# Kernel tuning notes

Measured on AMD Instinct MI355X. Metric: run time of the kernel, lower is better.

## Reference

```python
import jax, jax.numpy as jnp
import numpy as np
import math

EPS = 1e-7
N, M, K, D_IN, D_OUT = 8192, 32, 8, 64, 64
KP_EXTENT = 0.66

# ---- Lorentz manifold (curvature k = 1) helpers ----

def l_inner(x, y):
    # Lorentzian inner product, keepdim on last axis
    return -x[..., :1] * y[..., :1] + jnp.sum(x[..., 1:] * y[..., 1:], axis=-1, keepdims=True)

def l_dist(x, y):
    alpha = jnp.clip(-l_inner(x, y), 1.0 + EPS, None)
    return jnp.arccosh(alpha)[..., 0]

def expmap0(u):
    # u: tangent at origin, time component ignored-by-construction (zero)
    sp = u[..., 1:]
    un = jnp.sqrt(jnp.clip(jnp.sum(sp * sp, axis=-1, keepdims=True), 1e-14, None))
    return jnp.concatenate([jnp.cosh(un), jnp.sinh(un) * sp / un], axis=-1)

def expmap(x, u):
    un = jnp.sqrt(jnp.clip(l_inner(u, u), 1e-14, None))
    return jnp.cosh(un) * x + jnp.sinh(un) * u / un

def logmap(x, y):
    alpha = jnp.clip(-l_inner(x, y), 1.0 + EPS, None)
    d = jnp.arccosh(alpha)
    nom = y - alpha * x
    den = jnp.sqrt(jnp.clip(alpha * alpha - 1.0, 1e-14, None))
    return d * nom / den

def ptransp(x, y, v):
    # parallel transport of v from x to y
    return v + l_inner(y, v) / (1.0 - l_inner(x, y)) * (x + y)

def norm_midpoint(ave):
    den = jnp.sqrt(jnp.clip(jnp.abs(l_inner(ave, ave)), 1e-8, None))
    return ave / den


def setup_inputs() -> dict:
    key = jax.random.key(0)
    k1, k2, k3, k4, k5, k6 = jax.random.split(key, 6)
    # points on the hyperboloid: time = sqrt(1 + ||space||^2)
    sp = jax.random.normal(k1, (N, D_IN - 1), dtype=jnp.float32) * 0.5
    t = jnp.sqrt(1.0 + jnp.sum(sp * sp, axis=-1, keepdims=True))
    x = jnp.concatenate([t, sp], axis=-1)
    nei = jax.random.randint(k2, (N, M), 0, N, dtype=jnp.int32)
    nei_mask = jax.random.randint(k3, (N, M), 0, 2, dtype=jnp.int32)
    # kernel points: tangent vectors at origin (time comp 0), first point = center
    kp_sp = jax.random.normal(k4, (K, D_IN - 1), dtype=jnp.float32)
    kp_sp = kp_sp / jnp.linalg.norm(kp_sp, axis=-1, keepdims=True)
    radii = jax.random.uniform(k5, (K, 1), dtype=jnp.float32) * KP_EXTENT
    kp_sp = kp_sp * radii
    kp_sp = kp_sp.at[0].set(0.0)
    kernel_points = jnp.concatenate([jnp.zeros((K, 1), jnp.float32), kp_sp], axis=-1)
    # K LorentzLinear params
    stdv = 1.0 / math.sqrt(D_OUT)
    W = jax.random.uniform(k6, (K, D_OUT, D_IN), dtype=jnp.float32, minval=-stdv, maxval=stdv)
    W = W.at[:, :, 0].set(0.0)  # reset_parameters zeros first input column
    b = jnp.zeros((K, D_OUT), dtype=jnp.float32)
    scale = jnp.full((K,), math.log(10.0), dtype=jnp.float32)
    return {"x": x, "nei": nei, "nei_mask": nei_mask, "W": W, "b": b,
            "scale": scale, "kernel_points": kernel_points}


def reference(x, nei, nei_mask, W, b, scale, kernel_points):
    n, d = x.shape
    x_nei = x[nei]                      # [n, m, d] gather
    xr = x[:, None, :]                  # [n, 1, d]
    og_row = jnp.zeros((d,), x.dtype).at[0].set(1.0)
    # transport_x: map each neighborhood to the origin's tangent frame
    v = logmap(xr, x_nei)
    x0_nei = expmap0(ptransp(xr, og_row[None, None, :], v))   # [n, m, d]
    # kernel positions at the origin (transp=True => base point is origin)
    tmp = expmap(og_row[None, :], ptransp(og_row[None, :], og_row[None, :], kernel_points[1:]))
    x_kernel = jnp.concatenate([tmp, og_row[None, :]], axis=0)  # [K, d]
    # geodesic distances neighbor <-> kernel point: [n, K, m]
    dis = l_dist(x0_nei[:, None, :, :], x_kernel[None, :, None, :])
    dis = dis * nei_mask[:, None, :].astype(x.dtype)
    # K LorentzLinear transforms (vectorized over K): [n, K, m, d_out]
    h = jnp.einsum('nmd,kod->nkmo', x0_nei, W) + b[None, :, None, :]
    time = jax.nn.sigmoid(h[..., :1]) * jnp.exp(scale)[None, :, None, None] + 1.0001
    nar = h[..., 1:]
    s = (time * time - 1.0) / jnp.clip(jnp.sum(nar * nar, axis=-1, keepdims=True), 1e-8, None)
    xt = jnp.concatenate([time, nar * jnp.sqrt(s)], axis=-1)
    # weighted Lorentz midpoint over kernel points, per neighbor: [n, m, d_out]
    per_nei = norm_midpoint(jnp.einsum('nkm,nkmo->nmo', dis, xt))
    # unweighted Lorentz midpoint over neighbors: [n, d_out]
    return norm_midpoint(per_nei.mean(axis=1))
```

## Files before the change

### kernel.cpp

```cpp
#include <hip/hip_runtime.h>
#include <hip/hip_bf16.h>

#define N_NODES 8192
#define M_NEI   32
#define K_PTS   8
#define D       64
#define EPS_    1e-7f

typedef float f4v __attribute__((ext_vector_type(4)));
typedef short s8v __attribute__((ext_vector_type(8)));

__device__ __forceinline__ ushort f2bf(float f) {
  __hip_bfloat16 h = __float2bfloat16(f);
  return *reinterpret_cast<ushort*>(&h);
}
__device__ __forceinline__ float bf2f(ushort u) {
  __hip_bfloat16 h;
  *reinterpret_cast<ushort*>(&h) = u;
  return __bfloat162float(h);
}
__device__ __forceinline__ float frcp(float x)  { return __builtin_amdgcn_rcpf(x); }
__device__ __forceinline__ float frsq(float x)  { return __builtin_amdgcn_rsqf(x); }
__device__ __forceinline__ float fsqrt(float x) { return __builtin_amdgcn_sqrtf(x); }
__device__ __forceinline__ float facosh(float a) {
  float den = fsqrt(fmaxf(a * a - 1.f, 1e-14f));
  return __logf(a + den);
}

template<int CTRL>
__device__ __forceinline__ float dppadd(float v) {
  int t = __builtin_amdgcn_update_dpp(0, __float_as_int(v), CTRL, 0xf, 0xf, true);
  return v + __int_as_float(t);
}
template<int CTRL>
__device__ __forceinline__ float dppmov(float v) {
  return __int_as_float(__builtin_amdgcn_update_dpp(0, __float_as_int(v), CTRL, 0xf, 0xf, true));
}
__device__ __forceinline__ float swz_xor4(float v) {
  return __int_as_float(__builtin_amdgcn_ds_swizzle(__float_as_int(v), 0x101F));
}
__device__ __forceinline__ float sum8(float v) {
  v = dppadd<0xB1>(v);
  v = dppadd<0x4E>(v);
  v = dppadd<0x141>(v);
  return v;
}
__device__ __forceinline__ float sum16(float v) {
  v = dppadd<0x121>(v);
  v = dppadd<0x122>(v);
  v = dppadd<0x124>(v);
  v = dppadd<0x128>(v);
  return v;
}

__global__ void prep_xk(const float* __restrict__ kp, const float* __restrict__ scale,
                        float* __restrict__ xk) {
  int d = threadIdx.x;
  for (int kk = 0; kk < K_PTS - 1; ++kk) {
    float v = kp[(kk + 1) * D + d];
    float p = (d == 0) ? 0.f : v * v;
    #pragma unroll
    for (int s = 1; s < 64; s <<= 1) p += __shfl_xor(p, s);
    float un = sqrtf(fmaxf(p, 1e-14f));
    float sh = sinhf(un) / un;
    xk[kk * D + d] = (d == 0) ? coshf(un) : sh * v;
  }
  xk[(K_PTS - 1) * D + d] = (d == 0) ? 1.f : 0.f;
  if (d < K_PTS) xk[K_PTS * D + d] = expf(scale[d]);
}

__global__ void prep_wb(const float* __restrict__ W, ushort* __restrict__ WF) {
  int idx = blockIdx.x * 256 + threadIdx.x;
  int k    = idx >> 9;
  int ct   = (idx >> 7) & 3;
  int ks   = (idx >> 6) & 1;
  int lane = idx & 63;
  int o  = ct * 16 + (lane & 15);
  int db = (lane >> 4) * 8 + ks * 32;
  const float* wrow = W + (k * 64 + o) * 64 + db;
  s8v hi, lo;
  #pragma unroll
  for (int j = 0; j < 8; ++j) {
    float w = wrow[j];
    ushort h = f2bf(w);
    hi[j] = (short)h;
    lo[j] = (short)f2bf(w - bf2f(h));
  }
  int f = (k * 4 + ct) * 2 + ks;
  *(s8v*)(WF + (size_t)(f * 2 + 0) * 512 + lane * 8) = hi;
  *(s8v*)(WF + (size_t)(f * 2 + 1) * 512 + lane * 8) = lo;
}

__launch_bounds__(256, 4)
__global__ void kpa_main(const float* __restrict__ x, const int* __restrict__ nei,
                         const int* __restrict__ mask, const ushort* __restrict__ WF,
                         const float* __restrict__ b, const float* __restrict__ scale,
                         const float* __restrict__ xk, float* __restrict__ out) {
  __shared__ __align__(16) float  xr_s[D];
  __shared__ __align__(16) float  xk_s[K_PTS * D];
  __shared__ __align__(16) ushort Ah_lds[M_NEI * D];
  __shared__ __align__(16) ushort Al_lds[M_NEI * D];
  __shared__ float dis_s[K_PTS * 33];
  __shared__ __align__(8)  float  hss[K_PTS * M_NEI * 2];
  __shared__ __align__(16) float  red_h[2][16 * 68];
  __shared__ __align__(16) float  redp2[2][64];

  const int n  = blockIdx.x;
  const int t  = threadIdx.x;
  const int w4 = t >> 6;
  const int l  = t & 63;
  const int cl = l & 15;
  const int gr = l >> 4;
  const int wm = w4 & 1;
  const int wk = w4 >> 1;

  if (t < D) xr_s[t] = x[n * D + t];
  xk_s[t] = xk[t]; xk_s[t + 256] = xk[t + 256];
  __syncthreads();

  {
    const int m  = t >> 3;
    const int l8 = t & 7;
    const int d0 = l8 * 8;
    const int ni = nei[n * M_NEI + m];
    float y[8], xr[8];
    float y0 = x[ni * D];
    {
      float4 ya = *(const float4*)(x + ni * D + d0);
      float4 yb = *(const float4*)(x + ni * D + d0 + 4);
      y[0]=ya.x; y[1]=ya.y; y[2]=ya.z; y[3]=ya.w;
      y[4]=yb.x; y[5]=yb.y; y[6]=yb.z; y[7]=yb.w;
      float4 ra = *(const float4*)(xr_s + d0);
      float4 rb = *(const float4*)(xr_s + d0 + 4);
      xr[0]=ra.x; xr[1]=ra.y; xr[2]=ra.z; xr[3]=ra.w;
      xr[4]=rb.x; xr[5]=rb.y; xr[6]=rb.z; xr[7]=rb.w;
    }
    const float xr0 = xr_s[0];
    float p = 0.f;
    #pragma unroll
    for (int j = 0; j < 8; ++j) p += xr[j] * y[j];
    if (l8 == 0) p -= 2.f * xr[0] * y[0];
    p = sum8(p);
    float alpha = fmaxf(-p, 1.f + EPS_);
    float den = fsqrt(fmaxf(alpha * alpha - 1.f, 1e-14f));
    float dd  = __logf(alpha + den);
    float f   = dd * frcp(den);
    float v[8];
    #pragma unroll
    for (int j = 0; j < 8; ++j) v[j] = f * (y[j] - alpha * xr[j]);
    float v0 = f * (y0 - alpha * xr0);
    float c  = -v0 * frcp(1.f + xr0);
    float wv[8];
    float q = 0.f;
    #pragma unroll
    for (int j = 0; j < 8; ++j) { wv[j] = v[j] + c * xr[j]; q += wv[j] * wv[j]; }
    if (l8 == 0) q -= wv[0] * wv[0];
    q = sum8(q);
    float un = fsqrt(fmaxf(q, 1e-14f));
    float e  = __expf(un);
    float ei = frcp(e);
    float sh = (0.5f * (e - ei)) * frcp(un);
    float x0v[8];
    #pragma unroll
    for (int j = 0; j < 8; ++j) x0v[j] = sh * wv[j];
    if (l8 == 0) x0v[0] = 0.5f * (e + ei);
    {
      s8v hi, lo;
      #pragma unroll
      for (int j = 0; j < 8; ++j) {
        uint u = __float_as_uint(x0v[j]);
        hi[j] = (short)(ushort)(u >> 16);
        float lof = x0v[j] - __uint_as_float(u & 0xffff0000u);
        uint ul = __float_as_uint(lof);
        lo[j] = (short)(ushort)((ul + 0x7fffu + ((ul >> 16) & 1u)) >> 16);
      }
      int byte = m * 128 + d0 * 2;
      int swz  = byte ^ ((m & 7) << 4);
      *(s8v*)((char*)Ah_lds + swz) = hi;
      *(s8v*)((char*)Al_lds + swz) = lo;
    }
    float msk = (float)mask[n * M_NEI + m];
    if (l8 == 0) x0v[0] = -x0v[0];
    float pk[8];
    #pragma unroll
    for (int kk = 0; kk < K_PTS; ++kk) {
      const float* xkp = xk_s + kk * D + d0;
      float pp = 0.f;
      #pragma unroll
      for (int j = 0; j < 8; ++j) pp += x0v[j] * xkp[j];
      pk[kk] = pp;
    }
    const bool hi4 = (l8 & 4);
    float s1[4];
    #pragma unroll
    for (int j = 0; j < 4; ++j) {
      float give = hi4 ? pk[j] : pk[j + 4];
      float keep = hi4 ? pk[j + 4] : pk[j];
      s1[j] = keep + swz_xor4(give);
    }
    const bool hi2 = (l8 & 2);
    float s2[2];
    #pragma unroll
    for (int j = 0; j < 2; ++j) {
      float give = hi2 ? s1[j] : s1[j + 2];
      float keep = hi2 ? s1[j + 2] : s1[j];
      s2[j] = keep + dppmov<0x4E>(give);
    }
    const bool hi1 = (l8 & 1);
    float give = hi1 ? s2[0] : s2[1];
    float keep = hi1 ? s2[1] : s2[0];
    float mypp = keep + dppmov<0xB1>(give);
    float al_ = fmaxf(-mypp, 1.f + EPS_);
    dis_s[l8 * 33 + m] = facosh(al_) * msk;
  }
  __syncthreads();

  const int row = wm * 16 + cl;
  s8v ah[2], alo[2];
  #pragma unroll
  for (int ks = 0; ks < 2; ++ks) {
    int byte = row * 128 + (gr * 8 + ks * 32) * 2;
    int swz  = byte ^ ((row & 7) << 4);
    ah[ks]  = *(const s8v*)((const char*)Ah_lds + swz);
    alo[ks] = *(const s8v*)((const char*)Al_lds + swz);
  }

  f4v acc[4][4];
  #pragma unroll
  for (int kq = 0; kq < 4; ++kq) {
    const int k = wk * 4 + kq;
    #pragma unroll
    for (int ct = 0; ct < 4; ++ct) {
      float bv = b[k * 64 + ct * 16 + cl];
      f4v a = (f4v){bv, bv, bv, bv};
      #pragma unroll
      for (int ks = 0; ks < 2; ++ks) {
        int fi = (k * 4 + ct) * 2 + ks;
        s8v bh = *(const s8v*)(WF + (size_t)(fi * 2 + 0) * 512 + l * 8);
        s8v bl = *(const s8v*)(WF + (size_t)(fi * 2 + 1) * 512 + l * 8);
        a = __builtin_amdgcn_mfma_f32_16x16x32_bf16(ah[ks],  bh, a, 0, 0, 0);
        a = __builtin_amdgcn_mfma_f32_16x16x32_bf16(ah[ks],  bl, a, 0, 0, 0);
        a = __builtin_amdgcn_mfma_f32_16x16x32_bf16(alo[ks], bh, a, 0, 0, 0);
      }
      acc[kq][ct] = a;
    }
    #pragma unroll
    for (int r = 0; r < 4; ++r) {
      float ss = acc[kq][0][r]*acc[kq][0][r] + acc[kq][1][r]*acc[kq][1][r]
               + acc[kq][2][r]*acc[kq][2][r] + acc[kq][3][r]*acc[kq][3][r];
      ss = sum16(ss);
      if (cl == 0) {
        const int m = wm * 16 + gr * 4 + r;
        *(float2*)&hss[(k * M_NEI + m) * 2] = make_float2(acc[kq][0][r], ss);
      }
    }
  }
  __syncthreads();

  {
    const int k = t >> 5;
    const int m = t & 31;
    float2 hp = *(const float2*)&hss[(k * M_NEI + m) * 2];
    float h0 = hp.x, ss = hp.y;
    float nar2 = fmaxf(ss - h0 * h0, 1e-8f);
    float es   = xk[K_PTS * D + k];
    float time = es * frcp(1.f + __expf(-h0)) + 1.0001f;
    float sq   = fsqrt(time * time - 1.f) * frsq(nar2);
    float dm   = dis_s[k * 33 + m];
    *(float2*)&hss[(k * M_NEI + m) * 2] = make_float2(dm * sq, dm * time);
  }
  __syncthreads();

  float yacc[4][4];
  #pragma unroll
  for (int r = 0; r < 4; ++r)
    #pragma unroll
    for (int ct = 0; ct < 4; ++ct) yacc[r][ct] = 0.f;

  #pragma unroll
  for (int kq = 0; kq < 4; ++kq) {
    const int k = wk * 4 + kq;
    #pragma unroll
    for (int r = 0; r < 4; ++r) {
      const int m = wm * 16 + gr * 4 + r;
      float2 dd = *(const float2*)&hss[(k * M_NEI + m) * 2];
      yacc[r][0] += (cl == 0) ? dd.y : dd.x * acc[kq][0][r];
      yacc[r][1] += dd.x * acc[kq][1][r];
      yacc[r][2] += dd.x * acc[kq][2][r];
      yacc[r][3] += dd.x * acc[kq][3][r];
    }
  }

  if (wk == 1) {
    #pragma unroll
    for (int r = 0; r < 4; ++r) {
      const int ml = gr * 4 + r;
      float* rw = &red_h[wm][ml * 68];
      rw[cl]      = yacc[r][0];
      rw[16 + cl] = yacc[r][1];
      rw[32 + cl] = yacc[r][2];
      rw[48 + cl] = yacc[r][3];
    }
  }
  __syncthreads();

  if (wk == 0) {
    float s[4] = {0.f, 0.f, 0.f, 0.f};
    #pragma unroll
    for (int r = 0; r < 4; ++r) {
      const int ml = gr * 4 + r;
      const float* rw = &red_h[wm][ml * 68];
      float v0_ = yacc[r][0] + rw[cl];
      float v1_ = yacc[r][1] + rw[16 + cl];
      float v2_ = yacc[r][2] + rw[32 + cl];
      float v3_ = yacc[r][3] + rw[48 + cl];
      float ip = v0_*v0_ + v1_*v1_ + v2_*v2_ + v3_*v3_;
      if (cl == 0) ip -= 2.f * v0_ * v0_;
      ip = sum16(ip);
      float rin = frsq(fmaxf(fabsf(ip), 1e-8f));
      s[0] += v0_ * rin; s[1] += v1_ * rin;
      s[2] += v2_ * rin; s[3] += v3_ * rin;
    }
    #pragma unroll
    for (int j = 0; j < 4; ++j) {
      float z = s[j];
      z += __shfl_xor(z, 16); z += __shfl_xor(z, 32);
      s[j] = z;
    }
    if (gr == 0) {
      #pragma unroll
      for (int j = 0; j < 4; ++j) redp2[wm][j * 16 + cl] = s[j];
    }
  }
  __syncthreads();

  if (t < 16) {
    float mv[4]; float ip = 0.f;
    #pragma unroll
    for (int j = 0; j < 4; ++j) {
      mv[j] = (redp2[0][j * 16 + t] + redp2[1][j * 16 + t]) * (1.f / 32.f);
      ip += mv[j] * mv[j];
    }
    if (t == 0) ip -= 2.f * mv[0] * mv[0];
    ip = sum16(ip);
    float rin = frsq(fmaxf(fabsf(ip), 1e-8f));
    #pragma unroll
    for (int j = 0; j < 4; ++j) out[n * D + j * 16 + t] = mv[j] * rin;
  }
}

extern "C" void kernel_launch(void* const* d_in, const int* in_sizes, int n_in,
                              void* d_out, int out_size, void* d_ws, size_t ws_size,
                              hipStream_t stream) {
  const float* x     = (const float*)d_in[0];
  const int*   nei   = (const int*)d_in[1];
  const int*   mask  = (const int*)d_in[2];
  const float* W     = (const float*)d_in[3];
  const float* b     = (const float*)d_in[4];
  const float* scale = (const float*)d_in[5];
  const float* kp    = (const float*)d_in[6];
  float* out = (float*)d_out;

  ushort* WF = (ushort*)d_ws;
  float*  xk = (float*)(WF + 65536);

  prep_wb<<<16, 256, 0, stream>>>(W, WF);
  prep_xk<<<1, 64, 0, stream>>>(kp, scale, xk);
  kpa_main<<<N_NODES, 256, 0, stream>>>(x, nei, mask, WF, b, scale, xk, out);
}
```

Baseline: 103.0 us.

## Add per-kernel-point streamed variant with higher occupancy bound and runtime selection

Adds a second main kernel that processes the four kernel points per wave one at a time (non-unrolled loop) instead of holding all sixteen MFMA accumulators live. This lets it use launch bounds of 5 blocks per CU instead of 4. The host checks whether the new kernel compiled without register spills and launches it if so, otherwise falls back to the original. The trade is more occupancy against a serialized per-k loop that has less instruction-level parallelism. Each launch now also makes an extra host-side attribute query.

```diff
diff --git a/kernel.cpp b/kernel.cpp
--- a/kernel.cpp
+++ b/kernel.cpp
@@ -91,11 +91,168 @@
   *(s8v*)(WF + (size_t)(f * 2 + 1) * 512 + lane * 8) = lo;
 }
 
+#define KPA_PROLOGUE_AND_DIS                                                        \
+  if (t < D) xr_s[t] = x[n * D + t];                                                \
+  xk_s[t] = xk[t]; xk_s[t + 256] = xk[t + 256];                                     \
+  __syncthreads();                                                                  \
+  {                                                                                 \
+    const int m  = t >> 3;                                                          \
+    const int l8 = t & 7;                                                           \
+    const int d0 = l8 * 8;                                                          \
+    const int ni = nei[n * M_NEI + m];                                              \
+    float y[8], xr[8];                                                              \
+    float y0 = x[ni * D];                                                           \
+    {                                                                               \
+      float4 ya = *(const float4*)(x + ni * D + d0);                                \
+      float4 yb = *(const float4*)(x + ni * D + d0 + 4);                            \
+      y[0]=ya.x; y[1]=ya.y; y[2]=ya.z; y[3]=ya.w;                                   \
+      y[4]=yb.x; y[5]=yb.y; y[6]=yb.z; y[7]=yb.w;                                   \
+      float4 ra = *(const float4*)(xr_s + d0);                                      \
+      float4 rb = *(const float4*)(xr_s + d0 + 4);                                  \
+      xr[0]=ra.x; xr[1]=ra.y; xr[2]=ra.z; xr[3]=ra.w;                               \
+      xr[4]=rb.x; xr[5]=rb.y; xr[6]=rb.z; xr[7]=rb.w;                               \
+    }                                                                               \
+    const float xr0 = xr_s[0];                                                      \
+    float p = 0.f;                                                                  \
+    _Pragma("unroll")                                                               \
+    for (int j = 0; j < 8; ++j) p += xr[j] * y[j];                                  \
+    if (l8 == 0) p -= 2.f * xr[0] * y[0];                                           \
+    p = sum8(p);                                                                    \
+    float alpha = fmaxf(-p, 1.f + EPS_);                                            \
+    float den = fsqrt(fmaxf(alpha * alpha - 1.f, 1e-14f));                          \
+    float dd  = __logf(alpha + den);                                                \
+    float f   = dd * frcp(den);                                                     \
+    float v[8];                                                                     \
+    _Pragma("unroll")                                                               \
+    for (int j = 0; j < 8; ++j) v[j] = f * (y[j] - alpha * xr[j]);                  \
+    float v0 = f * (y0 - alpha * xr0);                                              \
+    float c  = -v0 * frcp(1.f + xr0);                                               \
+    float wv[8];                                                                    \
+    float q = 0.f;                                                                  \
+    _Pragma("unroll")                                                               \
+    for (int j = 0; j < 8; ++j) { wv[j] = v[j] + c * xr[j]; q += wv[j] * wv[j]; }   \
+    if (l8 == 0) q -= wv[0] * wv[0];                                                \
+    q = sum8(q);                                                                    \
+    float un = fsqrt(fmaxf(q, 1e-14f));                                             \
+    float e  = __expf(un);                                                          \
+    float ei = frcp(e);                                                             \
+    float sh = (0.5f * (e - ei)) * frcp(un);                                        \
+    float x0v[8];                                                                   \
+    _Pragma("unroll")                                                               \
+    for (int j = 0; j < 8; ++j) x0v[j] = sh * wv[j];                                \
+    if (l8 == 0) x0v[0] = 0.5f * (e + ei);                                          \
+    {                                                                               \
+      s8v hi, lo;                                                                   \
+      _Pragma("unroll")                                                             \
+      for (int j = 0; j < 8; ++j) {                                                 \
+        uint u = __float_as_uint(x0v[j]);                                           \
+        hi[j] = (short)(ushort)(u >> 16);                                           \
+        float lof = x0v[j] - __uint_as_float(u & 0xffff0000u);                      \
+        uint ul = __float_as_uint(lof);                                             \
+        lo[j] = (short)(ushort)((ul + 0x7fffu + ((ul >> 16) & 1u)) >> 16);          \
+      }                                                                             \
+      int byte = m * 128 + d0 * 2;                                                  \
+      int swz  = byte ^ ((m & 7) << 4);                                             \
+      *(s8v*)((char*)Ah_lds + swz) = hi;                                            \
+      *(s8v*)((char*)Al_lds + swz) = lo;                                            \
+    }                                                                               \
+    float msk = (float)mask[n * M_NEI + m];                                         \
+    if (l8 == 0) x0v[0] = -x0v[0];                                                  \
+    float pk[8];                                                                    \
+    _Pragma("unroll")                                                               \
+    for (int kk = 0; kk < K_PTS; ++kk) {                                            \
+      const float* xkp = xk_s + kk * D + d0;                                        \
+      float pp = 0.f;                                                               \
+      _Pragma("unroll")                                                             \
+      for (int j = 0; j < 8; ++j) pp += x0v[j] * xkp[j];                            \
+      pk[kk] = pp;                                                                  \
+    }                                                                               \
+    const bool hi4 = (l8 & 4);                                                      \
+    float s1[4];                                                                    \
+    _Pragma("unroll")                                                               \
+    for (int j = 0; j < 4; ++j) {                                                   \
+      float give = hi4 ? pk[j] : pk[j + 4];                                         \
+      float keep = hi4 ? pk[j + 4] : pk[j];                                         \
+      s1[j] = keep + swz_xor4(give);                                                \
+    }                                                                               \
+    const bool hi2 = (l8 & 2);                                                      \
+    float s2[2];                                                                    \
+    _Pragma("unroll")                                                               \
+    for (int j = 0; j < 2; ++j) {                                                   \
+      float give = hi2 ? s1[j] : s1[j + 2];                                         \
+      float keep = hi2 ? s1[j + 2] : s1[j];                                         \
+      s2[j] = keep + dppmov<0x4E>(give);                                            \
+    }                                                                               \
+    const bool hi1 = (l8 & 1);                                                      \
+    float give = hi1 ? s2[0] : s2[1];                                               \
+    float keep = hi1 ? s2[1] : s2[0];                                               \
+    float mypp = keep + dppmov<0xB1>(give);                                         \
+    float al_ = fmaxf(-mypp, 1.f + EPS_);                                           \
+    dis_s[l8 * 33 + m] = facosh(al_) * msk;                                         \
+  }                                                                                 \
+  __syncthreads();
+
+#define KPA_EPILOGUE                                                                \
+  if (wk == 1) {                                                                    \
+    _Pragma("unroll")                                                               \
+    for (int r = 0; r < 4; ++r) {                                                   \
+      const int ml = gr * 4 + r;                                                    \
+      float* rw = &red_h[wm][ml * 68];                                              \
+      rw[cl]      = yacc[r][0];                                                     \
+      rw[16 + cl] = yacc[r][1];                                                     \
+      rw[32 + cl] = yacc[r][2];                                                     \
+      rw[48 + cl] = yacc[r][3];                                                     \
+    }                                                                               \
+  }                                                                                 \
+  __syncthreads();                                                                  \
+  if (wk == 0) {                                                                    \
+    float s[4] = {0.f, 0.f, 0.f, 0.f};                                              \
+    _Pragma("unroll")                                                               \
+    for (int r = 0; r < 4; ++r) {                                                   \
+      const int ml = gr * 4 + r;                                                    \
+      const float* rw = &red_h[wm][ml * 68];                                        \
+      float v0_ = yacc[r][0] + rw[cl];                                              \
+      float v1_ = yacc[r][1] + rw[16 + cl];                                         \
+      float v2_ = yacc[r][2] + rw[32 + cl];                                         \
+      float v3_ = yacc[r][3] + rw[48 + cl];                                         \
+      float ip = v0_*v0_ + v1_*v1_ + v2_*v2_ + v3_*v3_;                             \
+      if (cl == 0) ip -= 2.f * v0_ * v0_;                                           \
+      ip = sum16(ip);                                                               \
+      float rin = frsq(fmaxf(fabsf(ip), 1e-8f));                                    \
+      s[0] += v0_ * rin; s[1] += v1_ * rin;                                         \
+      s[2] += v2_ * rin; s[3] += v3_ * rin;                                         \
+    }                                                                               \
+    _Pragma("unroll")                                                               \
+    for (int j = 0; j < 4; ++j) {                                                   \
+      float z = s[j];                                                               \
+      z += __shfl_xor(z, 16); z += __shfl_xor(z, 32);                               \
+      s[j] = z;                                                                     \
+    }                                                                               \
+    if (gr == 0) {                                                                  \
+      _Pragma("unroll")                                                             \
+      for (int j = 0; j < 4; ++j) redp2[wm][j * 16 + cl] = s[j];                    \
+    }                                                                               \
+  }                                                                                 \
+  __syncthreads();                                                                  \
+  if (t < 16) {                                                                     \
+    float mv[4]; float ip = 0.f;                                                    \
+    _Pragma("unroll")                                                               \
+    for (int j = 0; j < 4; ++j) {                                                   \
+      mv[j] = (redp2[0][j * 16 + t] + redp2[1][j * 16 + t]) * (1.f / 32.f);         \
+      ip += mv[j] * mv[j];                                                          \
+    }                                                                               \
+    if (t == 0) ip -= 2.f * mv[0] * mv[0];                                          \
+    ip = sum16(ip);                                                                 \
+    float rin = frsq(fmaxf(fabsf(ip), 1e-8f));                                      \
+    _Pragma("unroll")                                                               \
+    for (int j = 0; j < 4; ++j) out[n * D + j * 16 + t] = mv[j] * rin;              \
+  }
+
 __launch_bounds__(256, 4)
-__global__ void kpa_main(const float* __restrict__ x, const int* __restrict__ nei,
-                         const int* __restrict__ mask, const ushort* __restrict__ WF,
-                         const float* __restrict__ b, const float* __restrict__ scale,
-                         const float* __restrict__ xk, float* __restrict__ out) {
+__global__ void kpa_main4(const float* __restrict__ x, const int* __restrict__ nei,
+                          const int* __restrict__ mask, const ushort* __restrict__ WF,
+                          const float* __restrict__ b, const float* __restrict__ scale,
+                          const float* __restrict__ xk, float* __restrict__ out) {
   __shared__ __align__(16) float  xr_s[D];
   __shared__ __align__(16) float  xk_s[K_PTS * D];
   __shared__ __align__(16) ushort Ah_lds[M_NEI * D];
@@ -114,106 +271,7 @@
   const int wm = w4 & 1;
   const int wk = w4 >> 1;
 
-  if (t < D) xr_s[t] = x[n * D + t];
-  xk_s[t] = xk[t]; xk_s[t + 256] = xk[t + 256];
-  __syncthreads();
-
-  {
-    const int m  = t >> 3;
-    const int l8 = t & 7;
-    const int d0 = l8 * 8;
-    const int ni = nei[n * M_NEI + m];
-    float y[8], xr[8];
-    float y0 = x[ni * D];
-    {
-      float4 ya = *(const float4*)(x + ni * D + d0);
-      float4 yb = *(const float4*)(x + ni * D + d0 + 4);
-      y[0]=ya.x; y[1]=ya.y; y[2]=ya.z; y[3]=ya.w;
-      y[4]=yb.x; y[5]=yb.y; y[6]=yb.z; y[7]=yb.w;
-      float4 ra = *(const float4*)(xr_s + d0);
-      float4 rb = *(const float4*)(xr_s + d0 + 4);
-      xr[0]=ra.x; xr[1]=ra.y; xr[2]=ra.z; xr[3]=ra.w;
-      xr[4]=rb.x; xr[5]=rb.y; xr[6]=rb.z; xr[7]=rb.w;
-    }
-    const float xr0 = xr_s[0];
-    float p = 0.f;
-    #pragma unroll
-    for (int j = 0; j < 8; ++j) p += xr[j] * y[j];
-    if (l8 == 0) p -= 2.f * xr[0] * y[0];
-    p = sum8(p);
-    float alpha = fmaxf(-p, 1.f + EPS_);
-    float den = fsqrt(fmaxf(alpha * alpha - 1.f, 1e-14f));
-    float dd  = __logf(alpha + den);
-    float f   = dd * frcp(den);
-    float v[8];
-    #pragma unroll
-    for (int j = 0; j < 8; ++j) v[j] = f * (y[j] - alpha * xr[j]);
-    float v0 = f * (y0 - alpha * xr0);
-    float c  = -v0 * frcp(1.f + xr0);
-    float wv[8];
-    float q = 0.f;
-    #pragma unroll
-    for (int j = 0; j < 8; ++j) { wv[j] = v[j] + c * xr[j]; q += wv[j] * wv[j]; }
-    if (l8 == 0) q -= wv[0] * wv[0];
-    q = sum8(q);
-    float un = fsqrt(fmaxf(q, 1e-14f));
-    float e  = __expf(un);
-    float ei = frcp(e);
-    float sh = (0.5f * (e - ei)) * frcp(un);
-    float x0v[8];
-    #pragma unroll
-    for (int j = 0; j < 8; ++j) x0v[j] = sh * wv[j];
-    if (l8 == 0) x0v[0] = 0.5f * (e + ei);
-    {
-      s8v hi, lo;
-      #pragma unroll
-      for (int j = 0; j < 8; ++j) {
-        uint u = __float_as_uint(x0v[j]);
-        hi[j] = (short)(ushort)(u >> 16);
-        float lof = x0v[j] - __uint_as_float(u & 0xffff0000u);
-        uint ul = __float_as_uint(lof);
-        lo[j] = (short)(ushort)((ul + 0x7fffu + ((ul >> 16) & 1u)) >> 16);
-      }
-      int byte = m * 128 + d0 * 2;
-      int swz  = byte ^ ((m & 7) << 4);
-      *(s8v*)((char*)Ah_lds + swz) = hi;
-      *(s8v*)((char*)Al_lds + swz) = lo;
-    }
-    float msk = (float)mask[n * M_NEI + m];
-    if (l8 == 0) x0v[0] = -x0v[0];
-    float pk[8];
-    #pragma unroll
-    for (int kk = 0; kk < K_PTS; ++kk) {
-      const float* xkp = xk_s + kk * D + d0;
-      float pp = 0.f;
-      #pragma unroll
-      for (int j = 0; j < 8; ++j) pp += x0v[j] * xkp[j];
-      pk[kk] = pp;
-    }
-    const bool hi4 = (l8 & 4);
-    float s1[4];
-    #pragma unroll
-    for (int j = 0; j < 4; ++j) {
-      float give = hi4 ? pk[j] : pk[j + 4];
-      float keep = hi4 ? pk[j + 4] : pk[j];
-      s1[j] = keep + swz_xor4(give);
-    }
-    const bool hi2 = (l8 & 2);
-    float s2[2];
-    #pragma unroll
-    for (int j = 0; j < 2; ++j) {
-      float give = hi2 ? s1[j] : s1[j + 2];
-      float keep = hi2 ? s1[j + 2] : s1[j];
-      s2[j] = keep + dppmov<0x4E>(give);
-    }
-    const bool hi1 = (l8 & 1);
-    float give = hi1 ? s2[0] : s2[1];
-    float keep = hi1 ? s2[1] : s2[0];
-    float mypp = keep + dppmov<0xB1>(give);
-    float al_ = fmaxf(-mypp, 1.f + EPS_);
-    dis_s[l8 * 33 + m] = facosh(al_) * msk;
-  }
-  __syncthreads();
+  KPA_PROLOGUE_AND_DIS
 
   const int row = wm * 16 + cl;
   s8v ah[2], alo[2];
@@ -291,62 +349,104 @@
     }
   }
 
-  if (wk == 1) {
+  KPA_EPILOGUE
+}
+
+__launch_bounds__(256, 5)
+__global__ void kpa_main5(const float* __restrict__ x, const int* __restrict__ nei,
+                          const int* __restrict__ mask, const ushort* __restrict__ WF,
+                          const float* __restrict__ b, const float* __restrict__ scale,
+                          const float* __restrict__ xk, float* __restrict__ out) {
+  __shared__ __align__(16) float  xr_s[D];
+  __shared__ __align__(16) float  xk_s[K_PTS * D];
+  __shared__ __align__(16) ushort Ah_lds[M_NEI * D];
+  __shared__ __align__(16) ushort Al_lds[M_NEI * D];
+  __shared__ float dis_s[K_PTS * 33];
+  __shared__ __align__(8)  float  hss[K_PTS * M_NEI * 2];
+  __shared__ __align__(16) float  red_h[2][16 * 68];
+  __shared__ __align__(16) float  redp2[2][64];
+
+  const int n  = blockIdx.x;
+  const int t  = threadIdx.x;
+  const int w4 = t >> 6;
+  const int l  = t & 63;
+  const int cl = l & 15;
+  const int gr = l >> 4;
+  const int wm = w4 & 1;
+  const int wk = w4 >> 1;
+
+  KPA_PROLOGUE_AND_DIS
+
+  const int row = wm * 16 + cl;
+  s8v ah[2], alo[2];
+  #pragma unroll
+  for (int ks = 0; ks < 2; ++ks) {
+    int byte = row * 128 + (gr * 8 + ks * 32) * 2;
+    int swz  = byte ^ ((row & 7) << 4);
+    ah[ks]  = *(const s8v*)((const char*)Ah_lds + swz);
+    alo[ks] = *(const s8v*)((const char*)Al_lds + swz);
+  }
+
+  float yacc[4][4];
+  #pragma unroll
+  for (int r = 0; r < 4; ++r)
+    #pragma unroll
+    for (int ct = 0; ct < 4; ++ct) yacc[r][ct] = 0.f;
+
+  #pragma unroll 1
+  for (int kq = 0; kq < 4; ++kq) {
+    const int k = wk * 4 + kq;
+    f4v acc[4];
+    #pragma unroll
+    for (int ct = 0; ct < 4; ++ct) {
+      float bv = b[k * 64 + ct * 16 + cl];
+      f4v a = (f4v){bv, bv, bv, bv};
+      #pragma unroll
+      for (int ks = 0; ks < 2; ++ks) {
+        int fi = (k * 4 + ct) * 2 + ks;
+        s8v bh = *(const s8v*)(WF + (size_t)(fi * 2 + 0) * 512 + l * 8);
+        s8v bl = *(const s8v*)(WF + (size_t)(fi * 2 + 1) * 512 + l * 8);
+        a = __builtin_amdgcn_mfma_f32_16x16x32_bf16(ah[ks],  bh, a, 0, 0, 0);
+        a = __builtin_amdgcn_mfma_f32_16x16x32_bf16(ah[ks],  bl, a, 0, 0, 0);
+        a = __builtin_amdgcn_mfma_f32_16x16x32_bf16(alo[ks], bh, a, 0, 0, 0);
+      }
+      acc[ct] = a;
+    }
     #pragma unroll
     for (int r = 0; r < 4; ++r) {
-      const int ml = gr * 4 + r;
-      float* rw = &red_h[wm][ml * 68];
-      rw[cl]      = yacc[r][0];
-      rw[16 + cl] = yacc[r][1];
-      rw[32 + cl] = yacc[r][2];
-      rw[48 + cl] = yacc[r][3];
-    }
-  }
-  __syncthreads();
-
-  if (wk == 0) {
-    float s[4] = {0.f, 0.f, 0.f, 0.f};
+      float ss = acc[0][r]*acc[0][r] + acc[1][r]*acc[1][r]
+               + acc[2][r]*acc[2][r] + acc[3][r]*acc[3][r];
+      ss = sum16(ss);
+      if (cl == 0) {
+        const int m = wm * 16 + gr * 4 + r;
+        *(float2*)&hss[(k * M_NEI + m) * 2] = make_float2(acc[0][r], ss);
+      }
+    }
+    {
+      const float es = xk[K_PTS * D + k];
+      if (l < 16) {
+        const int mB = wm * 16 + l;
+        float2 hp = *(const float2*)&hss[(k * M_NEI + mB) * 2];
+        float h0 = hp.x, ss = hp.y;
+        float nar2 = fmaxf(ss - h0 * h0, 1e-8f);
+        float time = es * frcp(1.f + __expf(-h0)) + 1.0001f;
+        float sq   = fsqrt(time * time - 1.f) * frsq(nar2);
+        float dm   = dis_s[k * 33 + mB];
+        *(float2*)&hss[(k * M_NEI + mB) * 2] = make_float2(dm * sq, dm * time);
+      }
+    }
     #pragma unroll
     for (int r = 0; r < 4; ++r) {
-      const int ml = gr * 4 + r;
-      const float* rw = &red_h[wm][ml * 68];
-      float v0_ = yacc[r][0] + rw[cl];
-      float v1_ = yacc[r][1] + rw[16 + cl];
-      float v2_ = yacc[r][2] + rw[32 + cl];
-      float v3_ = yacc[r][3] + rw[48 + cl];
-      float ip = v0_*v0_ + v1_*v1_ + v2_*v2_ + v3_*v3_;
-      if (cl == 0) ip -= 2.f * v0_ * v0_;
-      ip = sum16(ip);
-      float rin = frsq(fmaxf(fabsf(ip), 1e-8f));
-      s[0] += v0_ * rin; s[1] += v1_ * rin;
-      s[2] += v2_ * rin; s[3] += v3_ * rin;
-    }
-    #pragma unroll
-    for (int j = 0; j < 4; ++j) {
-      float z = s[j];
-      z += __shfl_xor(z, 16); z += __shfl_xor(z, 32);
-      s[j] = z;
-    }
-    if (gr == 0) {
-      #pragma unroll
-      for (int j = 0; j < 4; ++j) redp2[wm][j * 16 + cl] = s[j];
-    }
-  }
-  __syncthreads();
-
-  if (t < 16) {
-    float mv[4]; float ip = 0.f;
-    #pragma unroll
-    for (int j = 0; j < 4; ++j) {
-      mv[j] = (redp2[0][j * 16 + t] + redp2[1][j * 16 + t]) * (1.f / 32.f);
-      ip += mv[j] * mv[j];
-    }
-    if (t == 0) ip -= 2.f * mv[0] * mv[0];
-    ip = sum16(ip);
-    float rin = frsq(fmaxf(fabsf(ip), 1e-8f));
-    #pragma unroll
-    for (int j = 0; j < 4; ++j) out[n * D + j * 16 + t] = mv[j] * rin;
-  }
+      const int m = wm * 16 + gr * 4 + r;
+      float2 dd = *(const float2*)&hss[(k * M_NEI + m) * 2];
+      yacc[r][0] += (cl == 0) ? dd.y : dd.x * acc[0][r];
+      yacc[r][1] += dd.x * acc[1][r];
+      yacc[r][2] += dd.x * acc[2][r];
+      yacc[r][3] += dd.x * acc[3][r];
+    }
+  }
+
+  KPA_EPILOGUE
 }
 
 extern "C" void kernel_launch(void* const* d_in, const int* in_sizes, int n_in,
@@ -366,5 +466,12 @@
 
   prep_wb<<<16, 256, 0, stream>>>(W, WF);
   prep_xk<<<1, 64, 0, stream>>>(kp, scale, xk);
-  kpa_main<<<N_NODES, 256, 0, stream>>>(x, nei, mask, WF, b, scale, xk, out);
-}
+
+  hipFuncAttributes a5;
+  bool use5 = (hipFuncGetAttributes(&a5, (const void*)kpa_main5) == hipSuccess)
+              && (a5.localSizeBytes == 0);
+  if (use5)
+    kpa_main5<<<N_NODES, 256, 0, stream>>>(x, nei, mask, WF, b, scale, xk, out);
+  else
+    kpa_main4<<<N_NODES, 256, 0, stream>>>(x, nei, mask, WF, b, scale, xk, out);
+}
```

After: 102.3 us. No clear change (-0.7%).
